# Kernel optimization log

Hardware: AMD Instinct MI355X
Metric: run time of the kernel (lower is better)

The kernel has to match this reference:

```python
import jax, jax.numpy as jnp
import numpy as np

TOPK = 8
EXTRA = 0  # ADDITIONAL_LAYERS_IN_GPU
CPU_TOPK = int(0.25 * 64)  # CPU_MOE_RATIO * num_experts = 16


def setup_inputs() -> dict:
    key = jax.random.key(0)
    k1, k2 = jax.random.split(key)
    hidden_states = jax.random.normal(k1, (4, 4096, 4096), dtype=jnp.float32)
    wg_weight = jax.random.normal(k2, (64, 4096), dtype=jnp.float32) * 0.02
    return {"hidden_states": hidden_states, "wg_weight": wg_weight}


def reference(hidden_states, wg_weight):
    bsz, seq_len, hidden_size = hidden_states.shape
    x = hidden_states.reshape(-1, hidden_size).astype(jnp.float32)  # [T, H]
    logits = jnp.einsum('th,eh->te', x, wg_weight)  # [T, 64]
    gates = jax.nn.softmax(logits, axis=1)
    values_all, indices_all = jax.lax.top_k(gates, TOPK + EXTRA)
    expert_weight = values_all[:, :TOPK]
    expert_index = indices_all[:, :TOPK]
    _, cpu_expert_index = jax.lax.top_k(gates, CPU_TOPK)
    cpu_expert_index = cpu_expert_index[:, 8 + EXTRA:]
    # norm_topk_prob=True, topk > 1
    eps = jnp.finfo(jnp.float32).eps
    denom = jnp.maximum(expert_weight.sum(axis=1, keepdims=True), eps)
    expert_weight = expert_weight / denom
    return (expert_weight, expert_index, cpu_expert_index, indices_all)
```

## Files before the change

kernel.cpp:

```cpp
#include <hip/hip_runtime.h>

#define T_TOK 16384
#define HDIM  4096
#define NEXP  64
#define TAU   2e-4f
#define BM    128

typedef unsigned short u16;
typedef u16   u16x8  __attribute__((ext_vector_type(8)));
typedef __bf16 bf16x8 __attribute__((ext_vector_type(8)));
typedef float f32x4  __attribute__((ext_vector_type(4)));

__device__ __forceinline__ u16 f2bf(float f) {
    unsigned u = __builtin_bit_cast(unsigned, f);
    unsigned r = u + 0x7FFFu + ((u >> 16) & 1u);
    return (u16)(r >> 16);
}
__device__ __forceinline__ float bf2f(u16 h) {
    unsigned u = ((unsigned)h) << 16;
    return __builtin_bit_cast(float, u);
}

__global__ void zero_counter(int* counter) {
    if (threadIdx.x == 0) counter[0] = 0;
}

__global__ __launch_bounds__(256)
void wsplit_kernel(const float* __restrict__ w, u16x8* __restrict__ wfrag,
                   float4* __restrict__ wt4) {
    const int id  = blockIdx.x * 256 + threadIdx.x;
    const int e   = id >> 9;
    const int k8g = id & 511;
    const int k   = k8g * 8;

    const float* wp = w + (size_t)e * HDIM + k;
    const float4 v0 = *(const float4*)wp;
    const float4 v1 = *(const float4*)(wp + 4);

    wt4[(size_t)(2 * k8g) * NEXP + e]     = v0;
    wt4[(size_t)(2 * k8g + 1) * NEXP + e] = v1;

    const float fv[8] = {v0.x, v0.y, v0.z, v0.w, v1.x, v1.y, v1.z, v1.w};
    u16x8 hv, lv;
#pragma unroll
    for (int j = 0; j < 8; ++j) {
        const u16 h = f2bf(fv[j]);
        hv[j] = h;
        lv[j] = f2bf(fv[j] - bf2f(h));
    }
    const int chunk = k >> 6;
    const int k8 = (k >> 3) & 7, ks = k8 >> 2, g = k8 & 3, nt = e >> 4;
    const int U = ks * 256 + nt * 64 + 16 * g + (e & 15);
    const int q = U ^ k8;
    wfrag[(size_t)chunk * 1024 + q]       = hv;
    wfrag[(size_t)chunk * 1024 + 512 + q] = lv;
}

__global__ __launch_bounds__(256, 3)
void gate_gemm_mfma(const float* __restrict__ x, const u16x8* __restrict__ wfrag,
                    float* __restrict__ partial, int ksplit) {
    const int b      = blockIdx.x;
    const int kslice = b % ksplit;
    const int tblk   = b / ksplit;
    const int kspan  = HDIM / ksplit;
    const int k0     = kslice * kspan;
    const int t0     = tblk * BM;

    __shared__ __align__(16) u16 smem[3072 * 8];

    const int tid  = threadIdx.x;
    const int lane = tid & 63;
    const int wv   = tid >> 6;

    f32x4 acc[2][4];
#pragma unroll
    for (int m = 0; m < 2; ++m)
#pragma unroll
        for (int nt = 0; nt < 4; ++nt) acc[m][nt] = (f32x4){0.f, 0.f, 0.f, 0.f};

    for (int kc = k0; kc < k0 + kspan; kc += 64) {
        const int chunkIdx = kc >> 6;
        __syncthreads();

        const u16x8* wsrc = wfrag + (size_t)chunkIdx * 1024;
#pragma unroll
        for (int i = 0; i < 4; ++i) {
            const int u = tid + 256 * i;
            *(u16x8*)(smem + (size_t)u * 8) = wsrc[u];
        }

#pragma unroll
        for (int i = 0; i < 4; ++i) {
            const int L   = tid + 256 * i;
            const int row = L >> 3;
            const int k8  = L & 7;
            const float* xp = x + (size_t)(t0 + row) * HDIM + kc + 8 * k8;
            const float4 v0 = *(const float4*)xp;
            const float4 v1 = *(const float4*)(xp + 4);
            const float fv[8] = {v0.x, v0.y, v0.z, v0.w, v1.x, v1.y, v1.z, v1.w};
            u16x8 hv, lv;
#pragma unroll
            for (int j = 0; j < 8; ++j) {
                const u16 h = f2bf(fv[j]);
                hv[j] = h;
                lv[j] = f2bf(fv[j] - bf2f(h));
            }
            const int g = k8 & 3, ks = k8 >> 2, mt = row >> 4;
            const int U = ks * 512 + mt * 64 + 16 * g + (row & 15);
            const int phys = U ^ k8;
            *(u16x8*)(smem + (size_t)(1024 + phys) * 8) = hv;
            *(u16x8*)(smem + (size_t)(2048 + phys) * 8) = lv;
        }
        __syncthreads();

#pragma unroll
        for (int ks = 0; ks < 2; ++ks) {
            const int xo = (ks << 2) + (lane >> 4);
            bf16x8 axh[2], axl[2];
#pragma unroll
            for (int m = 0; m < 2; ++m) {
                const int ux = (ks * 512 + (wv * 2 + m) * 64 + lane) ^ xo;
                axh[m] = __builtin_bit_cast(bf16x8, *(const u16x8*)(smem + (size_t)(1024 + ux) * 8));
                axl[m] = __builtin_bit_cast(bf16x8, *(const u16x8*)(smem + (size_t)(2048 + ux) * 8));
            }
#pragma unroll
            for (int nt = 0; nt < 4; ++nt) {
                const int uw = (ks * 256 + nt * 64 + lane) ^ xo;
                const bf16x8 bh = __builtin_bit_cast(bf16x8, *(const u16x8*)(smem + (size_t)uw * 8));
                const bf16x8 bl = __builtin_bit_cast(bf16x8, *(const u16x8*)(smem + (size_t)(512 + uw) * 8));
#pragma unroll
                for (int m = 0; m < 2; ++m) {
                    acc[m][nt] = __builtin_amdgcn_mfma_f32_16x16x32_bf16(axh[m], bh, acc[m][nt], 0, 0, 0);
                    acc[m][nt] = __builtin_amdgcn_mfma_f32_16x16x32_bf16(axh[m], bl, acc[m][nt], 0, 0, 0);
                    acc[m][nt] = __builtin_amdgcn_mfma_f32_16x16x32_bf16(axl[m], bh, acc[m][nt], 0, 0, 0);
                }
            }
        }
    }

    float* op = partial + (size_t)kslice * T_TOK * NEXP;
    const int ecol = lane & 15;
#pragma unroll
    for (int m = 0; m < 2; ++m) {
        const int trow = t0 + (wv * 2 + m) * 16 + ((lane >> 4) << 2);
#pragma unroll
        for (int nt = 0; nt < 4; ++nt)
#pragma unroll
            for (int r = 0; r < 4; ++r)
                op[(size_t)(trow + r) * NEXP + nt * 16 + ecol] = acc[m][nt][r];
    }
}

__global__ __launch_bounds__(256)
void gate_topk_f32(const float* __restrict__ partial, int ksplit,
                   float* __restrict__ out, int* __restrict__ list,
                   int* __restrict__ counter) {
    const int wave = threadIdx.x >> 6;
    const int lane = threadIdx.x & 63;
    const int t = blockIdx.x * 4 + wave;

    float l = 0.f;
    for (int s = 0; s < ksplit; ++s)
        l += partial[(size_t)s * T_TOK * NEXP + (size_t)t * NEXP + lane];

    float v = l;
    const int idx = lane;
    float myval = -3.4e38f;
    int   myidx = 0;
#pragma unroll
    for (int r = 0; r < 17; ++r) {
        float bv = v;
        int   bi = idx;
#pragma unroll
        for (int s = 1; s < 64; s <<= 1) {
            const float ov = __shfl_xor(bv, s);
            const int   oi = __shfl_xor(bi, s);
            if (ov > bv || (ov == bv && oi < bi)) { bv = ov; bi = oi; }
        }
        if (lane == r) { myval = bv; myidx = bi; }
        if (idx == bi) v = -3.4e38f;
    }

    const float nxt = __shfl(myval, (lane + 1) & 63);
    const bool close = (lane < 16) && (myval - nxt < TAU);
    if (__ballot(close) != 0ull) {
        if (lane == 0) { const int p = atomicAdd(counter, 1); list[p] = t; }
    }

    const float m = __shfl(myval, 0);
    const float p = (lane < 16) ? expf(myval - m) : 0.f;
    float s8 = (lane < 8) ? p : 0.f;
#pragma unroll
    for (int s = 1; s < 64; s <<= 1) s8 += __shfl_xor(s8, s);

    float* ew = out;
    float* ei = out + (size_t)T_TOK * 8;
    float* ci = out + (size_t)2 * T_TOK * 8;
    float* ia = out + (size_t)3 * T_TOK * 8;
    if (lane < 8) {
        ew[(size_t)t * 8 + lane] = p / s8;
        ei[(size_t)t * 8 + lane] = (float)myidx;
        ia[(size_t)t * 8 + lane] = (float)myidx;
    } else if (lane < 16) {
        ci[(size_t)t * 8 + (lane - 8)] = (float)myidx;
    }
}

__global__ __launch_bounds__(256)
void gate_repair_f64(const float* __restrict__ x, const float4* __restrict__ wt4,
                     const int* __restrict__ list, const int* __restrict__ counter,
                     float* __restrict__ out) {
    const int lane = threadIdx.x & 63;
    const int wid  = (int)((blockIdx.x * blockDim.x + threadIdx.x) >> 6);
    const int nw   = (int)((gridDim.x * blockDim.x) >> 6);
    const int n    = counter[0];

    for (int i = wid; i < n; i += nw) {
        const int t = __builtin_amdgcn_readfirstlane(list[i]);
        const float4* xr4 = (const float4*)(x + (size_t)t * HDIM);

        double a0 = 0.0, a1 = 0.0, a2 = 0.0, a3 = 0.0;
        for (int k4 = 0; k4 < HDIM / 4; k4 += 4) {
            const float4 w0 = wt4[(size_t)(k4 + 0) * NEXP + lane];
            const float4 w1 = wt4[(size_t)(k4 + 1) * NEXP + lane];
            const float4 w2 = wt4[(size_t)(k4 + 2) * NEXP + lane];
            const float4 w3 = wt4[(size_t)(k4 + 3) * NEXP + lane];
            const float4 x0 = xr4[k4 + 0];
            const float4 x1 = xr4[k4 + 1];
            const float4 x2 = xr4[k4 + 2];
            const float4 x3 = xr4[k4 + 3];
            a0 = fma((double)x0.x, (double)w0.x, a0);
            a0 = fma((double)x0.y, (double)w0.y, a0);
            a0 = fma((double)x0.z, (double)w0.z, a0);
            a0 = fma((double)x0.w, (double)w0.w, a0);
            a1 = fma((double)x1.x, (double)w1.x, a1);
            a1 = fma((double)x1.y, (double)w1.y, a1);
            a1 = fma((double)x1.z, (double)w1.z, a1);
            a1 = fma((double)x1.w, (double)w1.w, a1);
            a2 = fma((double)x2.x, (double)w2.x, a2);
            a2 = fma((double)x2.y, (double)w2.y, a2);
            a2 = fma((double)x2.z, (double)w2.z, a2);
            a2 = fma((double)x2.w, (double)w2.w, a2);
            a3 = fma((double)x3.x, (double)w3.x, a3);
            a3 = fma((double)x3.y, (double)w3.y, a3);
            a3 = fma((double)x3.z, (double)w3.z, a3);
            a3 = fma((double)x3.w, (double)w3.w, a3);
        }
        double v = (a0 + a1) + (a2 + a3);

        const int idx = lane;
        double mylog = -1.0e308;
        int    myidx = 0;
#pragma unroll
        for (int r = 0; r < 16; ++r) {
            double bv = v;
            int    bi = idx;
#pragma unroll
            for (int s = 1; s < 64; s <<= 1) {
                const double ov = __shfl_xor(bv, s);
                const int    oi = __shfl_xor(bi, s);
                if (ov > bv || (ov == bv && oi < bi)) { bv = ov; bi = oi; }
            }
            if (lane == r) { mylog = bv; myidx = bi; }
            if (idx == bi) v = -1.0e308;
        }

        const double m = __shfl(mylog, 0);
        const float p = (lane < 16) ? expf((float)(mylog - m)) : 0.f;
        float s8 = (lane < 8) ? p : 0.f;
#pragma unroll
        for (int s = 1; s < 64; s <<= 1) s8 += __shfl_xor(s8, s);

        float* ew = out;
        float* ei = out + (size_t)T_TOK * 8;
        float* ci = out + (size_t)2 * T_TOK * 8;
        float* ia = out + (size_t)3 * T_TOK * 8;
        if (lane < 8) {
            ew[(size_t)t * 8 + lane] = p / s8;
            ei[(size_t)t * 8 + lane] = (float)myidx;
            ia[(size_t)t * 8 + lane] = (float)myidx;
        } else if (lane < 16) {
            ci[(size_t)t * 8 + (lane - 8)] = (float)myidx;
        }
    }
}

extern "C" void kernel_launch(void* const* d_in, const int* in_sizes, int n_in,
                              void* d_out, int out_size, void* d_ws, size_t ws_size,
                              hipStream_t stream) {
    const float* x = (const float*)d_in[0];
    const float* w = (const float*)d_in[1];
    float* out     = (float*)d_out;

    const size_t slice      = (size_t)T_TOK * NEXP * sizeof(float);
    const size_t wfragBytes = (size_t)64 * 1024 * 16;
    const size_t wt4Bytes   = (size_t)NEXP * HDIM * sizeof(float);
    const size_t extra      = wfragBytes + wt4Bytes + (size_t)T_TOK * sizeof(int) + 64;

    int ksplit = 1;
    if      (ws_size >= 4 * slice + extra) ksplit = 4;
    else if (ws_size >= 2 * slice + extra) ksplit = 2;

    float*  partial = (float*)d_ws;
    u16x8*  wfrag   = (u16x8*)((char*)d_ws + (size_t)ksplit * slice);
    float4* wt4     = (float4*)((char*)wfrag + wfragBytes);
    int*    list    = (int*)((char*)wt4 + wt4Bytes);
    int*    counter = list + T_TOK;

    zero_counter<<<1, 64, 0, stream>>>(counter);
    wsplit_kernel<<<128, 256, 0, stream>>>(w, wfrag, wt4);
    gate_gemm_mfma<<<ksplit * (T_TOK / BM), 256, 0, stream>>>(x, wfrag, partial, ksplit);
    gate_topk_f32<<<T_TOK / 4, 256, 0, stream>>>(partial, ksplit, out, list, counter);
    gate_repair_f64<<<256, 256, 0, stream>>>(x, wt4, list, counter, out);
}
```

Measured before the change: 188.1 us.

## Prefetch next GEMM chunk into registers and split f64 repair along K

The GEMM main loop now issues the global loads for the next 64-wide K chunk into registers before the compute phase, so load latency overlaps the MFMA work of the current chunk. The f64 repair pass is split into a partial kernel that spreads each flagged token's dot product over 16 K-slices across many more waves, and a final kernel that sums the slices and does the top-k. This trades extra registers in the GEMM and a large f64 scratch buffer plus one more launch for more parallelism in the repair stage. The larger workspace requirement may also push ksplit down if ws_size is limited.

```diff
diff --git a/kernel.cpp b/kernel.cpp
--- a/kernel.cpp
+++ b/kernel.cpp
@@ -78,26 +78,36 @@
 #pragma unroll
         for (int nt = 0; nt < 4; ++nt) acc[m][nt] = (f32x4){0.f, 0.f, 0.f, 0.f};
 
+    u16x8  wreg[4];
+    float4 xr0[4], xr1[4];
+
+    auto issue = [&](int kc) {
+        const u16x8* ws = wfrag + (size_t)(kc >> 6) * 1024;
+#pragma unroll
+        for (int i = 0; i < 4; ++i) wreg[i] = ws[tid + 256 * i];
+#pragma unroll
+        for (int i = 0; i < 4; ++i) {
+            const int L = tid + 256 * i;
+            const int row = L >> 3, k8 = L & 7;
+            const float* xp = x + (size_t)(t0 + row) * HDIM + kc + 8 * k8;
+            xr0[i] = *(const float4*)xp;
+            xr1[i] = *(const float4*)(xp + 4);
+        }
+    };
+
+    issue(k0);
+
     for (int kc = k0; kc < k0 + kspan; kc += 64) {
-        const int chunkIdx = kc >> 6;
         __syncthreads();
 
-        const u16x8* wsrc = wfrag + (size_t)chunkIdx * 1024;
+#pragma unroll
+        for (int i = 0; i < 4; ++i)
+            *(u16x8*)(smem + (size_t)(tid + 256 * i) * 8) = wreg[i];
 #pragma unroll
         for (int i = 0; i < 4; ++i) {
-            const int u = tid + 256 * i;
-            *(u16x8*)(smem + (size_t)u * 8) = wsrc[u];
-        }
-
-#pragma unroll
-        for (int i = 0; i < 4; ++i) {
-            const int L   = tid + 256 * i;
-            const int row = L >> 3;
-            const int k8  = L & 7;
-            const float* xp = x + (size_t)(t0 + row) * HDIM + kc + 8 * k8;
-            const float4 v0 = *(const float4*)xp;
-            const float4 v1 = *(const float4*)(xp + 4);
-            const float fv[8] = {v0.x, v0.y, v0.z, v0.w, v1.x, v1.y, v1.z, v1.w};
+            const int L = tid + 256 * i, row = L >> 3, k8 = L & 7;
+            const float fv[8] = {xr0[i].x, xr0[i].y, xr0[i].z, xr0[i].w,
+                                 xr1[i].x, xr1[i].y, xr1[i].z, xr1[i].w};
             u16x8 hv, lv;
 #pragma unroll
             for (int j = 0; j < 8; ++j) {
@@ -111,6 +121,9 @@
             *(u16x8*)(smem + (size_t)(1024 + phys) * 8) = hv;
             *(u16x8*)(smem + (size_t)(2048 + phys) * 8) = lv;
         }
+
+        if (kc + 64 < k0 + kspan) issue(kc + 64);
+
         __syncthreads();
 
 #pragma unroll
@@ -207,28 +220,32 @@
 }
 
 __global__ __launch_bounds__(256)
-void gate_repair_f64(const float* __restrict__ x, const float4* __restrict__ wt4,
-                     const int* __restrict__ list, const int* __restrict__ counter,
-                     float* __restrict__ out) {
+void repair_partial(const float* __restrict__ x, const float4* __restrict__ wt4,
+                    const int* __restrict__ list, const int* __restrict__ counter,
+                    double* __restrict__ fpart) {
     const int lane = threadIdx.x & 63;
     const int wid  = (int)((blockIdx.x * blockDim.x + threadIdx.x) >> 6);
     const int nw   = (int)((gridDim.x * blockDim.x) >> 6);
-    const int n    = counter[0];
-
-    for (int i = wid; i < n; i += nw) {
-        const int t = __builtin_amdgcn_readfirstlane(list[i]);
-        const float4* xr4 = (const float4*)(x + (size_t)t * HDIM);
+    const int nit  = counter[0] * 16;
+
+    for (int it = wid; it < nit; it += nw) {
+        const int li = it >> 4;
+        const int ks = it & 15;
+        const int t  = __builtin_amdgcn_readfirstlane(list[li]);
+        const float4* xr4 = (const float4*)(x + (size_t)t * HDIM) + ks * 64;
+        const float4* wb  = wt4 + (size_t)ks * 64 * NEXP;
 
         double a0 = 0.0, a1 = 0.0, a2 = 0.0, a3 = 0.0;
-        for (int k4 = 0; k4 < HDIM / 4; k4 += 4) {
-            const float4 w0 = wt4[(size_t)(k4 + 0) * NEXP + lane];
-            const float4 w1 = wt4[(size_t)(k4 + 1) * NEXP + lane];
-            const float4 w2 = wt4[(size_t)(k4 + 2) * NEXP + lane];
-            const float4 w3 = wt4[(size_t)(k4 + 3) * NEXP + lane];
-            const float4 x0 = xr4[k4 + 0];
-            const float4 x1 = xr4[k4 + 1];
-            const float4 x2 = xr4[k4 + 2];
-            const float4 x3 = xr4[k4 + 3];
+#pragma unroll 4
+        for (int j = 0; j < 64; j += 4) {
+            const float4 w0 = wb[(size_t)(j + 0) * NEXP + lane];
+            const float4 w1 = wb[(size_t)(j + 1) * NEXP + lane];
+            const float4 w2 = wb[(size_t)(j + 2) * NEXP + lane];
+            const float4 w3 = wb[(size_t)(j + 3) * NEXP + lane];
+            const float4 x0 = xr4[j + 0];
+            const float4 x1 = xr4[j + 1];
+            const float4 x2 = xr4[j + 2];
+            const float4 x3 = xr4[j + 3];
             a0 = fma((double)x0.x, (double)w0.x, a0);
             a0 = fma((double)x0.y, (double)w0.y, a0);
             a0 = fma((double)x0.z, (double)w0.z, a0);
@@ -246,7 +263,25 @@
             a3 = fma((double)x3.z, (double)w3.z, a3);
             a3 = fma((double)x3.w, (double)w3.w, a3);
         }
-        double v = (a0 + a1) + (a2 + a3);
+        fpart[(size_t)li * 1024 + ks * 64 + lane] = (a0 + a1) + (a2 + a3);
+    }
+}
+
+__global__ __launch_bounds__(256)
+void repair_final(const double* __restrict__ fpart, const int* __restrict__ list,
+                  const int* __restrict__ counter, float* __restrict__ out) {
+    const int lane = threadIdx.x & 63;
+    const int wid  = (int)((blockIdx.x * blockDim.x + threadIdx.x) >> 6);
+    const int nw   = (int)((gridDim.x * blockDim.x) >> 6);
+    const int n    = counter[0];
+
+    for (int li = wid; li < n; li += nw) {
+        const int t = __builtin_amdgcn_readfirstlane(list[li]);
+
+        double v = 0.0;
+#pragma unroll
+        for (int ks = 0; ks < 16; ++ks)
+            v += fpart[(size_t)li * 1024 + ks * 64 + lane];
 
         const int idx = lane;
         double mylog = -1.0e308;
@@ -295,7 +330,9 @@
     const size_t slice      = (size_t)T_TOK * NEXP * sizeof(float);
     const size_t wfragBytes = (size_t)64 * 1024 * 16;
     const size_t wt4Bytes   = (size_t)NEXP * HDIM * sizeof(float);
-    const size_t extra      = wfragBytes + wt4Bytes + (size_t)T_TOK * sizeof(int) + 64;
+    const size_t fpartBytes = (size_t)T_TOK * 16 * NEXP * sizeof(double);
+    const size_t extra      = wfragBytes + wt4Bytes + fpartBytes +
+                              (size_t)T_TOK * sizeof(int) + 64;
 
     int ksplit = 1;
     if      (ws_size >= 4 * slice + extra) ksplit = 4;
@@ -304,12 +341,14 @@
     float*  partial = (float*)d_ws;
     u16x8*  wfrag   = (u16x8*)((char*)d_ws + (size_t)ksplit * slice);
     float4* wt4     = (float4*)((char*)wfrag + wfragBytes);
-    int*    list    = (int*)((char*)wt4 + wt4Bytes);
+    double* fpart   = (double*)((char*)wt4 + wt4Bytes);
+    int*    list    = (int*)((char*)fpart + fpartBytes);
     int*    counter = list + T_TOK;
 
     zero_counter<<<1, 64, 0, stream>>>(counter);
     wsplit_kernel<<<128, 256, 0, stream>>>(w, wfrag, wt4);
     gate_gemm_mfma<<<ksplit * (T_TOK / BM), 256, 0, stream>>>(x, wfrag, partial, ksplit);
     gate_topk_f32<<<T_TOK / 4, 256, 0, stream>>>(partial, ksplit, out, list, counter);
-    gate_repair_f64<<<256, 256, 0, stream>>>(x, wt4, list, counter, out);
-}
+    repair_partial<<<4096, 256, 0, stream>>>(x, wt4, list, counter, fpart);
+    repair_final<<<1024, 256, 0, stream>>>(fpart, list, counter, out);
+}
```

After: 155.2 us. 17.5% less time.
